# Optimization experiments

Hardware: AMD Instinct MI355X
Metric: run time of the kernel (lower is better)

Reference implementation:

```python
import jax, jax.numpy as jnp
import numpy as np

B, P, K, HE, HF = 256, 128, 512, 1024, 512
D = K + HE + 2 * HF  # 2560, MLP input dim
HID = 64


def setup_inputs() -> dict:
    key = jax.random.key(0)
    ks = jax.random.split(key, 6)
    query = jax.random.normal(ks[0], (B, 1, HE), dtype=jnp.float32)
    keys = jax.random.normal(ks[1], (B, P, K), dtype=jnp.float32)
    frameLSTM_h = jax.random.normal(ks[2], (B, 1, 2 * HF), dtype=jnp.float32)
    mask = jax.random.randint(ks[3], (B, P), 0, 2, dtype=jnp.int32)
    mask = mask.at[:, 0].set(1)  # guarantee at least one unmasked player per row
    W1 = jax.random.normal(ks[4], (D, HID), dtype=jnp.float32) / np.float32(np.sqrt(D))
    W2 = jax.random.normal(ks[5], (HID, 1), dtype=jnp.float32) / np.float32(np.sqrt(HID))
    return dict(query=query, keys=keys, frameLSTM_h=frameLSTM_h, mask=mask, W1=W1, W2=W2)


def reference(query, keys, frameLSTM_h, mask, W1, W2):
    # Faithful to: cat([keys, query.repeat, frame.repeat]) @ W1 -> ReLU -> @ W2.
    # The pre-activation is linear, so splitting W1 by row-blocks is exactly the
    # same math without materializing the repeated/concatenated (B,P,D) tensor.
    W1k = W1[:K]            # (K, 64)
    W1q = W1[K:K + HE]      # (HE, 64)
    W1f = W1[K + HE:]       # (2*HF, 64)
    h = jax.nn.relu(
        jnp.einsum('bpk,kh->bph', keys, W1k)
        + jnp.einsum('boe,eh->boh', query, W1q)        # broadcasts over P
        + jnp.einsum('bof,fh->boh', frameLSTM_h, W1f)  # broadcasts over P
    )  # (B, P, 64)
    raw_scores = jnp.einsum('bph,ho->bp', h, W2)  # (B, P)
    raw_scores = jnp.where(mask == 0, -jnp.inf, raw_scores)
    weights = jax.nn.softmax(raw_scores, axis=1)  # (B, P)
    context = jnp.einsum('bp,bpk->bk', weights, keys)[:, None, :]  # (B, 1, K)
    embeddings = jnp.concatenate([context, frameLSTM_h], axis=2)   # (B, 1, K+2*HF)
    return embeddings, weights
```

## Files before the change

kernel.cpp:

```cpp
#include <hip/hip_runtime.h>
#include <hip/hip_bf16.h>
#include <cstdint>
#include <math.h>


typedef __bf16 bf16;
typedef __attribute__((ext_vector_type(8))) __bf16 bf16x8;
typedef __attribute__((ext_vector_type(4))) float f32x4;

#define NB 256
#define NP 128
#define NK 512

__global__ __launch_bounds__(512) void prep_kernel(
    const float* __restrict__ W1, const float* __restrict__ query,
    const float* __restrict__ frame, bf16* __restrict__ w1kt,
    float* __restrict__ proj)
{
    __shared__ float s[64][65];
    __shared__ float sq[4][2048];
    __shared__ float red[8][4][64];
    const int blk = blockIdx.x;
    const int t = threadIdx.x;
    if (blk < 8) {
        const int k0 = blk * 64;
#pragma unroll
        for (int i = 0; i < 8; i++) {
            const int idx = t + 512 * i;
            const int k = idx >> 6, h = idx & 63;
            s[k][h] = W1[(size_t)(k0 + k) * 64 + h];
        }
        __syncthreads();
#pragma unroll
        for (int i = 0; i < 8; i++) {
            const int idx = t + 512 * i;
            const int h = idx >> 6, kk = idx & 63;
            w1kt[(size_t)h * 512 + k0 + kk] = (bf16)s[kk][h];
        }
    } else {
        const int b0 = (blk - 8) * 4;
#pragma unroll
        for (int i = 0; i < 4; i++) {
            const int flat = (t + 512 * i) * 4;
            const int bl = flat >> 11;
            const int d  = flat & 2047;
            const float* src = (d < 1024)
                ? (query + (size_t)(b0 + bl) * 1024 + d)
                : (frame + (size_t)(b0 + bl) * 1024 + (d - 1024));
            *(float4*)&sq[bl][d] = *(const float4*)src;
        }
        __syncthreads();

        const int w = t >> 6;
        const int h = t & 63;
        const float* w1c = W1 + (size_t)(512 + w * 256) * 64 + h;
        float wreg[4][16];
#pragma unroll
        for (int bu = 0; bu < 3; bu++)
#pragma unroll
            for (int u = 0; u < 16; u++)
                wreg[bu][u] = w1c[(size_t)(bu * 16 + u) * 64];

        float acc[4] = {0.f, 0.f, 0.f, 0.f};
#pragma unroll
        for (int rr = 0; rr < 16; rr++) {
            const int cur = rr & 3;
            if (rr < 13) {
#pragma unroll
                for (int u = 0; u < 16; u++)
                    wreg[(rr + 3) & 3][u] = w1c[(size_t)((rr + 3) * 16 + u) * 64];
            }
#pragma unroll
            for (int u4 = 0; u4 < 4; u4++) {
                float4 qv[4];
#pragma unroll
                for (int j = 0; j < 4; j++)
                    qv[j] = *(const float4*)&sq[j][w * 256 + rr * 16 + u4 * 4];
#pragma unroll
                for (int uu = 0; uu < 4; uu++) {
                    const float wv = wreg[cur][u4 * 4 + uu];
                    acc[0] += (&qv[0].x)[uu] * wv;
                    acc[1] += (&qv[1].x)[uu] * wv;
                    acc[2] += (&qv[2].x)[uu] * wv;
                    acc[3] += (&qv[3].x)[uu] * wv;
                }
            }
        }
#pragma unroll
        for (int j = 0; j < 4; j++) red[w][j][h] = acc[j];
        __syncthreads();
        if (t < 256) {
            const int j2 = t >> 6, hh = t & 63;
            float sum = 0.f;
#pragma unroll
            for (int ww = 0; ww < 8; ww++) sum += red[ww][j2][hh];
            proj[(size_t)(b0 + j2) * 64 + hh] = sum;
        }
    }
}

__global__ __launch_bounds__(256, 2) void scores_kernel(
    const float* __restrict__ keys, const float* __restrict__ W2,
    const bf16* __restrict__ w1kt, const float* __restrict__ proj,
    float* __restrict__ sws)
{
    const int blk = blockIdx.x;
    const int b = blk >> 1;
    const int ph = blk & 1;
    const int t = threadIdx.x;
    const int w = t >> 6;
    const int lane = t & 63;
    const int m = lane & 15;
    const int q = lane >> 4;
    const int p0 = ph * 64 + w * 16;

    float pv[4], wv[4];
#pragma unroll
    for (int nt = 0; nt < 4; nt++) {
        pv[nt] = proj[b * 64 + nt * 16 + m];
        wv[nt] = W2[nt * 16 + m];
    }

    const float* arow = keys + (size_t)b * (NP * NK) + (size_t)(p0 + m) * NK + q * 8;
    const bf16* bb = w1kt + m * 512 + q * 8;

    f32x4 acc[4];
#pragma unroll
    for (int nt = 0; nt < 4; nt++) acc[nt] = (f32x4){0.f, 0.f, 0.f, 0.f};

    float4 Aa[2], Ab[2];
    bf16x8 Bp[2][4];
    Aa[0] = *(const float4*)(arow);
    Ab[0] = *(const float4*)(arow + 4);
#pragma unroll
    for (int nt = 0; nt < 4; nt++) Bp[0][nt] = *(const bf16x8*)(bb + nt * 8192);

#pragma unroll
    for (int kk = 0; kk < 16; kk++) {
        const int cur = kk & 1;
        if (kk < 15) {
            Aa[cur ^ 1] = *(const float4*)(arow + (kk + 1) * 32);
            Ab[cur ^ 1] = *(const float4*)(arow + (kk + 1) * 32 + 4);
#pragma unroll
            for (int nt = 0; nt < 4; nt++)
                Bp[cur ^ 1][nt] = *(const bf16x8*)(bb + nt * 8192 + (kk + 1) * 32);
        }
        bf16x8 Af;
        Af[0] = (bf16)Aa[cur].x; Af[1] = (bf16)Aa[cur].y;
        Af[2] = (bf16)Aa[cur].z; Af[3] = (bf16)Aa[cur].w;
        Af[4] = (bf16)Ab[cur].x; Af[5] = (bf16)Ab[cur].y;
        Af[6] = (bf16)Ab[cur].z; Af[7] = (bf16)Ab[cur].w;
#pragma unroll
        for (int nt = 0; nt < 4; nt++)
            acc[nt] = __builtin_amdgcn_mfma_f32_16x16x32_bf16(Af, Bp[cur][nt], acc[nt], 0, 0, 0);
    }

    float pr[4] = {0.f, 0.f, 0.f, 0.f};
#pragma unroll
    for (int nt = 0; nt < 4; nt++)
#pragma unroll
        for (int r = 0; r < 4; r++)
            pr[r] += fmaxf(acc[nt][r] + pv[nt], 0.f) * wv[nt];

#pragma unroll
    for (int off = 1; off < 16; off <<= 1)
#pragma unroll
        for (int r = 0; r < 4; r++)
            pr[r] += __shfl_xor(pr[r], off);

    if (m == 0) {
#pragma unroll
        for (int r = 0; r < 4; r++)
            sws[(size_t)b * 128 + p0 + q * 4 + r] = pr[r];
    }
}

__global__ __launch_bounds__(512, 2) void ctx_kernel(
    const float* __restrict__ keys, const float* __restrict__ frame,
    const int* __restrict__ mask, const float* __restrict__ sws,
    float* __restrict__ out)
{
    __shared__ float wts[128];
    const int b = blockIdx.x;
    const int t = threadIdx.x;

    if (t < 64) {
        const int pa = t, pb = t + 64;
        float s0 = (mask[b * 128 + pa] == 0) ? -INFINITY : sws[(size_t)b * 128 + pa];
        float s1 = (mask[b * 128 + pb] == 0) ? -INFINITY : sws[(size_t)b * 128 + pb];
        float mx = fmaxf(s0, s1);
#pragma unroll
        for (int off = 32; off; off >>= 1) mx = fmaxf(mx, __shfl_xor(mx, off));
        float e0 = __expf(s0 - mx), e1 = __expf(s1 - mx);
        float sum = e0 + e1;
#pragma unroll
        for (int off = 32; off; off >>= 1) sum += __shfl_xor(sum, off);
        const float inv = 1.0f / sum;
        e0 *= inv; e1 *= inv;
        wts[pa] = e0; wts[pb] = e1;
        float* wout = out + (size_t)NB * 1536;
        wout[b * 128 + pa] = e0;
        wout[b * 128 + pb] = e1;
    }
    __syncthreads();

    const float* kc = keys + (size_t)b * (NP * NK) + t;
    float kreg[2][16];
#pragma unroll
    for (int i = 0; i < 16; i++) kreg[0][i] = kc[(size_t)i * NK];
    float acc = 0.f;
#pragma unroll
    for (int c8 = 0; c8 < 8; c8++) {
        const int cur = c8 & 1;
        if (c8 < 7) {
#pragma unroll
            for (int i = 0; i < 16; i++)
                kreg[cur ^ 1][i] = kc[(size_t)((c8 + 1) * 16 + i) * NK];
        }
#pragma unroll
        for (int i = 0; i < 16; i++)
            acc += wts[c8 * 16 + i] * kreg[cur][i];
    }
    out[(size_t)b * 1536 + t] = acc;

    if (t < 256) {
        const float4 fv = *(const float4*)(frame + (size_t)b * 1024 + t * 4);
        *(float4*)(out + (size_t)b * 1536 + 512 + t * 4) = fv;
    }
}

extern "C" void kernel_launch(void* const* d_in, const int* in_sizes, int n_in,
                              void* d_out, int out_size, void* d_ws, size_t ws_size,
                              hipStream_t stream) {
    const float* query = (const float*)d_in[0];
    const float* keys  = (const float*)d_in[1];
    const float* frame = (const float*)d_in[2];
    const int*   mask  = (const int*)d_in[3];
    const float* W1    = (const float*)d_in[4];
    const float* W2    = (const float*)d_in[5];
    float* out = (float*)d_out;

    bf16* w1kt  = (bf16*)d_ws;
    float* proj = (float*)((char*)d_ws + (64 << 10));
    float* sws  = (float*)((char*)d_ws + (128 << 10));

    prep_kernel<<<72, 512, 0, stream>>>(W1, query, frame, w1kt, proj);
    scores_kernel<<<512, 256, 0, stream>>>(keys, W2, w1kt, proj, sws);
    ctx_kernel<<<256, 512, 0, stream>>>(keys, frame, mask, sws, out);
}
```

Before: 140.7 us.

## Stage W1k^T into swizzled LDS per block and deepen keys prefetch

The scores kernel now has each block copy the full bf16 W1k^T (64 KB) into dynamic shared memory with an XOR swizzle, then reads B operands from LDS instead of global memory. The keys A-operand prefetch is deepened from double to quadruple buffering (3 tiles ahead). This aims to cut repeated global/L2 loads of the weight matrix and hide keys latency better. The cost is 64 KB LDS per block, which limits occupancy, plus an extra 64 KB copy and a barrier in every one of 512 blocks.

```diff
diff --git a/kernel.cpp b/kernel.cpp
--- a/kernel.cpp
+++ b/kernel.cpp
@@ -99,11 +99,12 @@
     }
 }
 
-__global__ __launch_bounds__(256, 2) void scores_kernel(
+__global__ __launch_bounds__(256) void scores_kernel(
     const float* __restrict__ keys, const float* __restrict__ W2,
     const bf16* __restrict__ w1kt, const float* __restrict__ proj,
     float* __restrict__ sws)
 {
+    extern __shared__ char sB[];
     const int blk = blockIdx.x;
     const int b = blk >> 1;
     const int ph = blk & 1;
@@ -113,6 +114,26 @@
     const int m = lane & 15;
     const int q = lane >> 4;
     const int p0 = ph * 64 + w * 16;
+    const int xorv = (m & 7) << 4;
+
+    const float* arow = keys + (size_t)b * (NP * NK) + (size_t)(p0 + m) * NK + q * 8;
+
+    float4 Aa[4], Ab[4];
+#pragma unroll
+    for (int i = 0; i < 3; i++) {
+        Aa[i] = *(const float4*)(arow + i * 32);
+        Ab[i] = *(const float4*)(arow + i * 32 + 4);
+    }
+
+    {
+        const char* wsrc = (const char*)w1kt;
+#pragma unroll
+        for (int i = 0; i < 16; i++) {
+            const int o = t * 256 + i * 16;
+            const int row = o >> 10;
+            *(bf16x8*)(sB + (o ^ ((row & 7) << 4))) = *(const bf16x8*)(wsrc + o);
+        }
+    }
 
     float pv[4], wv[4];
 #pragma unroll
@@ -120,30 +141,30 @@
         pv[nt] = proj[b * 64 + nt * 16 + m];
         wv[nt] = W2[nt * 16 + m];
     }
-
-    const float* arow = keys + (size_t)b * (NP * NK) + (size_t)(p0 + m) * NK + q * 8;
-    const bf16* bb = w1kt + m * 512 + q * 8;
+    __syncthreads();
 
     f32x4 acc[4];
 #pragma unroll
     for (int nt = 0; nt < 4; nt++) acc[nt] = (f32x4){0.f, 0.f, 0.f, 0.f};
 
-    float4 Aa[2], Ab[2];
     bf16x8 Bp[2][4];
-    Aa[0] = *(const float4*)(arow);
-    Ab[0] = *(const float4*)(arow + 4);
-#pragma unroll
-    for (int nt = 0; nt < 4; nt++) Bp[0][nt] = *(const bf16x8*)(bb + nt * 8192);
+#pragma unroll
+    for (int nt = 0; nt < 4; nt++)
+        Bp[0][nt] = *(const bf16x8*)(sB + nt * 16384 + m * 1024 + ((q * 16) ^ xorv));
 
 #pragma unroll
     for (int kk = 0; kk < 16; kk++) {
-        const int cur = kk & 1;
+        const int cur = kk & 3;
+        const int bc = kk & 1;
+        if (kk < 13) {
+            Aa[(kk + 3) & 3] = *(const float4*)(arow + (kk + 3) * 32);
+            Ab[(kk + 3) & 3] = *(const float4*)(arow + (kk + 3) * 32 + 4);
+        }
         if (kk < 15) {
-            Aa[cur ^ 1] = *(const float4*)(arow + (kk + 1) * 32);
-            Ab[cur ^ 1] = *(const float4*)(arow + (kk + 1) * 32 + 4);
 #pragma unroll
             for (int nt = 0; nt < 4; nt++)
-                Bp[cur ^ 1][nt] = *(const bf16x8*)(bb + nt * 8192 + (kk + 1) * 32);
+                Bp[bc ^ 1][nt] = *(const bf16x8*)(sB + nt * 16384 + m * 1024
+                                  + ((((kk + 1) * 64) | (q * 16)) ^ xorv));
         }
         bf16x8 Af;
         Af[0] = (bf16)Aa[cur].x; Af[1] = (bf16)Aa[cur].y;
@@ -152,7 +173,7 @@
         Af[6] = (bf16)Ab[cur].z; Af[7] = (bf16)Ab[cur].w;
 #pragma unroll
         for (int nt = 0; nt < 4; nt++)
-            acc[nt] = __builtin_amdgcn_mfma_f32_16x16x32_bf16(Af, Bp[cur][nt], acc[nt], 0, 0, 0);
+            acc[nt] = __builtin_amdgcn_mfma_f32_16x16x32_bf16(Af, Bp[bc][nt], acc[nt], 0, 0, 0);
     }
 
     float pr[4] = {0.f, 0.f, 0.f, 0.f};
@@ -244,7 +265,10 @@
     float* proj = (float*)((char*)d_ws + (64 << 10));
     float* sws  = (float*)((char*)d_ws + (128 << 10));
 
+    hipFuncSetAttribute((const void*)scores_kernel,
+                        hipFuncAttributeMaxDynamicSharedMemorySize, 65536);
+
     prep_kernel<<<72, 512, 0, stream>>>(W1, query, frame, w1kt, proj);
-    scores_kernel<<<512, 256, 0, stream>>>(keys, W2, w1kt, proj, sws);
+    scores_kernel<<<512, 256, 65536, stream>>>(keys, W2, w1kt, proj, sws);
     ctx_kernel<<<256, 512, 0, stream>>>(keys, frame, mask, sws, out);
 }
```

Measured after the change: 130.6 us. 7.1% less time.
